# Optimization experiments

Hardware: AMD Instinct MI355X
Metric: run time of the kernel (lower is better)

Reference implementation:

```python
import jax, jax.numpy as jnp
import numpy as np

N_EDGES = 1048576
N_CENTERS = 32768
N_SPECIES = 4
L_MAX = 3
N_BASIS = 12
N_MAX = 8
R_CUT = 5.0
NORM = 1.0 / np.sqrt(32.0)  # hypers['normalize'] = avg_num_neighbors = 32
SH_SPLITS = [0, 1, 4, 9, 16]  # cumulative offsets of (2l+1)


def real_sph_harm_lmax3(u):
    # u: [E,3] unit vectors; returns [E,16] real normalized spherical harmonics (sphericart order m=-l..l)
    x, y, z = u[:, 0], u[:, 1], u[:, 2]
    c0 = 0.5 * np.sqrt(1.0 / np.pi)
    c1 = np.sqrt(3.0 / (4.0 * np.pi))
    x2, y2, z2 = x * x, y * y, z * z
    sh = [
        jnp.full_like(x, c0),
        c1 * y, c1 * z, c1 * x,
        0.5 * np.sqrt(15.0 / np.pi) * x * y,
        0.5 * np.sqrt(15.0 / np.pi) * y * z,
        0.25 * np.sqrt(5.0 / np.pi) * (3.0 * z2 - 1.0),
        0.5 * np.sqrt(15.0 / np.pi) * x * z,
        0.25 * np.sqrt(15.0 / np.pi) * (x2 - y2),
        0.25 * np.sqrt(35.0 / (2.0 * np.pi)) * y * (3.0 * x2 - y2),
        0.5 * np.sqrt(105.0 / np.pi) * x * y * z,
        0.25 * np.sqrt(21.0 / (2.0 * np.pi)) * y * (5.0 * z2 - 1.0),
        0.25 * np.sqrt(7.0 / np.pi) * (5.0 * z2 * z - 3.0 * z),
        0.25 * np.sqrt(21.0 / (2.0 * np.pi)) * x * (5.0 * z2 - 1.0),
        0.25 * np.sqrt(105.0 / np.pi) * z * (x2 - y2),
        0.25 * np.sqrt(35.0 / (2.0 * np.pi)) * x * (x2 - y2),
    ]
    return jnp.stack(sh, axis=1)


def setup_inputs() -> dict:
    key = jax.random.key(0)
    k1, k2, k3, k4 = jax.random.split(key, 4)
    vectors = jax.random.normal(k1, (N_EDGES, 3), dtype=jnp.float32) * 1.5
    radial_weights = jax.random.normal(k2, (L_MAX + 1, N_BASIS, N_MAX), dtype=jnp.float32) * 0.1
    center_index = jax.random.randint(k3, (N_EDGES,), 0, N_CENTERS, dtype=jnp.int64)
    neighbor_species_index = jax.random.randint(k4, (N_EDGES,), 0, N_SPECIES, dtype=jnp.int64)
    return {"vectors": vectors, "radial_weights": radial_weights,
            "center_index": center_index, "neighbor_species_index": neighbor_species_index}


def reference(vectors, radial_weights, center_index, neighbor_species_index):
    # distances and unit vectors
    r = jnp.sqrt(jnp.sum(vectors * vectors, axis=-1) + 1e-12)  # [E]
    u = vectors / r[:, None]
    # smooth radial basis phi_n(r) = sin((n+1) pi r / r_cut)/r, normalized (LE-like)
    ns = jnp.arange(1, N_BASIS + 1, dtype=vectors.dtype)
    phi = jnp.sin(np.pi / R_CUT * r[:, None] * ns[None, :]) / r[:, None] * NORM  # [E, N_BASIS]
    sh = real_sph_harm_lmax3(u)  # [E,16]
    # scatter target: (center, neighbor_species) channel
    idx = center_index * N_SPECIES + neighbor_species_index  # [E]
    densities = []
    for l in range(L_MAX + 1):
        m_l = 2 * l + 1
        sh_l = jax.lax.slice_in_dim(sh, SH_SPLITS[l], SH_SPLITS[l + 1], axis=1)  # [E, 2l+1]
        rad_l = phi @ radial_weights[l]  # [E, N_MAX]
        edge_l = rad_l[:, None, :] * sh_l[:, :, None]  # [E, 2l+1, N_MAX] outer product
        dens = jax.ops.segment_sum(edge_l.reshape(edge_l.shape[0], -1), idx,
                                   num_segments=N_CENTERS * N_SPECIES)  # [N*S, m*n]
        dens = dens.reshape(N_CENTERS, N_SPECIES, m_l, N_MAX)
        dens = jnp.transpose(dens, (0, 2, 1, 3)).reshape(N_CENTERS, m_l, N_SPECIES * N_MAX)
        densities.append(dens)  # c^{a_i l}_{Ai, m, a_j n}
    # concatenate the per-l TensorMap blocks along the m axis -> [N, sum(2l+1), S*N_MAX]
    return jnp.concatenate(densities, axis=1)
```

## Files before the change

### kernel.cpp

```cpp
#include <hip/hip_runtime.h>
#include <math.h>

#define N_EDGES   1048576
#define N_BUCKET  1024
#define SEG_PER_B 128
#define N_BASIS   12
#define CAP       2048

#define WS_COUNTS   0
#define WS_OFFSETS  4096
#define WS_CURSORS  8192
#define WS_SORTED   12288
#define WS_NEEDED   (12288 + 4194304)

__device__ __forceinline__ void compute_edge(float x, float y, float z,
                                             float* __restrict__ ph,
                                             float* __restrict__ sh)
{
    const float r2    = fmaf(x, x, fmaf(y, y, z * z)) + 1e-12f;
    const float inv_r = rsqrtf(r2);
    const float r     = r2 * inv_r;
    x *= inv_r; y *= inv_r; z *= inv_r;

    const float t = 0.6283185307179586f * r;
    float s1, c1;
    __sincosf(t, &s1, &c1);
    const float twoc = 2.0f * c1;
    const float scale = 0.17677669529663687f * inv_r;
    float skm1 = 0.0f, sk = s1;
    #pragma unroll
    for (int b = 0; b < N_BASIS; ++b) {
        ph[b] = sk * scale;
        const float nxt = fmaf(twoc, sk, -skm1);
        skm1 = sk; sk = nxt;
    }

    const float x2 = x * x, y2 = y * y, z2 = z * z;
    sh[0]  = 0.28209479177387814f;
    sh[1]  = 0.4886025119029199f * y;
    sh[2]  = 0.4886025119029199f * z;
    sh[3]  = 0.4886025119029199f * x;
    sh[4]  = 1.0925484305920792f * x * y;
    sh[5]  = 1.0925484305920792f * y * z;
    sh[6]  = 0.31539156525252005f * (3.0f * z2 - 1.0f);
    sh[7]  = 1.0925484305920792f * x * z;
    sh[8]  = 0.5462742152960396f * (x2 - y2);
    sh[9]  = 0.5900435899266435f * y * (3.0f * x2 - y2);
    sh[10] = 2.890611442640554f  * x * y * z;
    sh[11] = 0.4570457994644658f * y * (5.0f * z2 - 1.0f);
    sh[12] = 0.3731763325901154f * (5.0f * z2 * z - 3.0f * z);
    sh[13] = 0.4570457994644658f * x * (5.0f * z2 - 1.0f);
    sh[14] = 1.445305721320277f  * z * (x2 - y2);
    sh[15] = 0.5900435899266435f * x * (x2 - y2);
}

__device__ __forceinline__ void flush_seg(const float* __restrict__ acc,
                                          int b, int sl, int n,
                                          float* __restrict__ out)
{
    const int seg = b * SEG_PER_B + sl;
    float* op = out + (size_t)(seg >> 2) * 512 + (seg & 3) * 8 + n;
    #pragma unroll
    for (int L = 0; L < 16; ++L) op[L * 32] = acc[L];
}

__global__ __launch_bounds__(256) void hist_kernel(
    const int* __restrict__ cidx, const int* __restrict__ sidx,
    int* __restrict__ counts)
{
    __shared__ int h[N_BUCKET];
    const int t = threadIdx.x;
    #pragma unroll
    for (int i = t; i < N_BUCKET; i += 256) h[i] = 0;
    __syncthreads();
    const int base = blockIdx.x * 4096;
    #pragma unroll
    for (int k = 0; k < 16; ++k) {
        const int e = base + k * 256 + t;
        const int seg = (cidx[e] << 2) | sidx[e];
        atomicAdd(&h[seg >> 7], 1);
    }
    __syncthreads();
    #pragma unroll
    for (int i = t; i < N_BUCKET; i += 256)
        if (h[i]) atomicAdd(&counts[i], h[i]);
}

__global__ __launch_bounds__(1024) void scan_kernel(
    const int* __restrict__ counts, int* __restrict__ offsets,
    int* __restrict__ cursors)
{
    __shared__ int tmp[N_BUCKET];
    const int t = threadIdx.x;
    const int orig = counts[t];
    tmp[t] = orig;
    __syncthreads();
    #pragma unroll
    for (int d = 1; d < N_BUCKET; d <<= 1) {
        const int v = (t >= d) ? tmp[t - d] : 0;
        __syncthreads();
        tmp[t] += v;
        __syncthreads();
    }
    const int off = tmp[t] - orig;
    offsets[t] = off;
    cursors[t] = off;
}

__global__ __launch_bounds__(256) void partition_kernel(
    const int* __restrict__ cidx, const int* __restrict__ sidx,
    int* __restrict__ cursors, unsigned int* __restrict__ sorted_rec)
{
    __shared__ int bhist[N_BUCKET];
    __shared__ int bbase[N_BUCKET];
    __shared__ int lcnt[N_BUCKET];
    const int t = threadIdx.x;
    #pragma unroll
    for (int i = t; i < N_BUCKET; i += 256) bhist[i] = 0;
    __syncthreads();

    const int base = blockIdx.x * 4096;
    int segs[16];
    #pragma unroll
    for (int k = 0; k < 16; ++k) {
        const int e = base + k * 256 + t;
        segs[k] = (cidx[e] << 2) | sidx[e];
        atomicAdd(&bhist[segs[k] >> 7], 1);
    }
    __syncthreads();

    #pragma unroll
    for (int i = t; i < N_BUCKET; i += 256) {
        const int c = bhist[i];
        if (c) bbase[i] = atomicAdd(&cursors[i], c);
        lcnt[i] = 0;
    }
    __syncthreads();

    #pragma unroll
    for (int k = 0; k < 16; ++k) {
        const int e = base + k * 256 + t;
        const int seg = segs[k];
        const int bkt = seg >> 7;
        const int pos = bbase[bkt] + atomicAdd(&lcnt[bkt], 1);
        sorted_rec[pos] = ((unsigned)(seg & 127) << 20) | (unsigned)e;
    }
}

__global__ __launch_bounds__(256) void compute_kernel(
    const unsigned int* __restrict__ sorted_rec,
    const int* __restrict__ offsets, const int* __restrict__ counts,
    const float* __restrict__ vectors,
    const float* __restrict__ rw,
    float* __restrict__ out)
{
    __shared__ float4 pay[CAP];
    __shared__ int shist[SEG_PER_B];
    __shared__ int soff[SEG_PER_B];
    __shared__ int scur[SEG_PER_B];

    const int t = threadIdx.x;
    const int b = blockIdx.x;
    const int n = t & 7;
    const int g = t >> 3;

    float Wn[4][N_BASIS];
    #pragma unroll
    for (int l = 0; l < 4; ++l)
        #pragma unroll
        for (int bb = 0; bb < N_BASIS; ++bb)
            Wn[l][bb] = rw[(l * N_BASIS + bb) * 8 + n];

    const int off = offsets[b];
    const int cnt = counts[b];

    if (cnt > CAP) {
        #pragma unroll 1
        for (int k = 0; k < 4; ++k) {
            const int sl = g * 4 + k;
            float acc[16];
            #pragma unroll
            for (int L = 0; L < 16; ++L) acc[L] = 0.0f;
            for (int j = 0; j < cnt; ++j) {
                const unsigned rec = sorted_rec[off + j];
                if ((int)(rec >> 20) != sl) continue;
                const int eid = rec & 0xFFFFF;
                float ph[N_BASIS], sh[16];
                compute_edge(vectors[3*eid], vectors[3*eid+1], vectors[3*eid+2], ph, sh);
                float rad[4];
                #pragma unroll
                for (int l = 0; l < 4; ++l) {
                    float a = 0.0f;
                    #pragma unroll
                    for (int bb = 0; bb < N_BASIS; ++bb)
                        a = fmaf(ph[bb], Wn[l][bb], a);
                    rad[l] = a;
                }
                #pragma unroll
                for (int L = 0; L < 16; ++L) {
                    const int l = (L == 0) ? 0 : (L < 4) ? 1 : (L < 9) ? 2 : 3;
                    acc[L] = fmaf(sh[L], rad[l], acc[L]);
                }
            }
            flush_seg(acc, b, sl, n, out);
        }
        return;
    }

    if (t < SEG_PER_B) shist[t] = 0;
    __syncthreads();

    unsigned recs[8];
    const int iters = (cnt + 255) >> 8;
    #pragma unroll
    for (int it = 0; it < 8; ++it) {
        const int i = it * 256 + t;
        if (it < iters && i < cnt) {
            recs[it] = sorted_rec[off + i];
            atomicAdd(&shist[recs[it] >> 20], 1);
        }
    }
    __syncthreads();

    if (t < SEG_PER_B) soff[t] = shist[t];
    __syncthreads();
    #pragma unroll
    for (int d = 1; d < SEG_PER_B; d <<= 1) {
        int v = 0;
        if (t >= d && t < SEG_PER_B) v = soff[t - d];
        __syncthreads();
        if (t < SEG_PER_B) soff[t] += v;
        __syncthreads();
    }
    if (t < SEG_PER_B) {
        const int ex = soff[t] - shist[t];
        soff[t] = ex;
        scur[t] = ex;
    }
    __syncthreads();

    #pragma unroll
    for (int it = 0; it < 8; ++it) {
        const int i = it * 256 + t;
        if (it < iters && i < cnt) {
            const unsigned rec = recs[it];
            const int sl  = rec >> 20;
            const int eid = rec & 0xFFFFF;
            const int r = atomicAdd(&scur[sl], 1);
            pay[r] = make_float4(vectors[3 * eid], vectors[3 * eid + 1],
                                 vectors[3 * eid + 2], __int_as_float(sl));
        }
    }
    __syncthreads();

    const int s0 = g * 4;
    const int js = soff[s0];
    const int je = (s0 + 4 < SEG_PER_B) ? soff[s0 + 4] : cnt;

    int cur = -1;
    float acc[16];
    #pragma unroll
    for (int L = 0; L < 16; ++L) acc[L] = 0.0f;

    for (int j = js; j < je; ++j) {
        const float4 v = pay[j];
        const int sl = __float_as_int(v.w);
        if (sl != cur) {
            if (cur >= 0) {
                flush_seg(acc, b, cur, n, out);
                #pragma unroll
                for (int L = 0; L < 16; ++L) acc[L] = 0.0f;
            }
            cur = sl;
        }
        float ph[N_BASIS], sh[16];
        compute_edge(v.x, v.y, v.z, ph, sh);
        float rad[4];
        #pragma unroll
        for (int l = 0; l < 4; ++l) {
            float a = 0.0f;
            #pragma unroll
            for (int bb = 0; bb < N_BASIS; ++bb)
                a = fmaf(ph[bb], Wn[l][bb], a);
            rad[l] = a;
        }
        #pragma unroll
        for (int L = 0; L < 16; ++L) {
            const int l = (L == 0) ? 0 : (L < 4) ? 1 : (L < 9) ? 2 : 3;
            acc[L] = fmaf(sh[L], rad[l], acc[L]);
        }
    }
    if (cur >= 0) flush_seg(acc, b, cur, n, out);

    #pragma unroll
    for (int k = 0; k < 4; ++k) {
        const int sl = s0 + k;
        if (shist[sl] == 0) {
            float z[16];
            #pragma unroll
            for (int L = 0; L < 16; ++L) z[L] = 0.0f;
            flush_seg(z, b, sl, n, out);
        }
    }
}

__global__ __launch_bounds__(256) void atomic_kernel(
    const float* __restrict__ vectors, const float* __restrict__ rw,
    const int* __restrict__ cidx, const int* __restrict__ sidx,
    float* __restrict__ out)
{
    const int e = blockIdx.x * 256 + threadIdx.x;
    if (e >= N_EDGES) return;
    float ph[N_BASIS], sh[16];
    compute_edge(vectors[3*e], vectors[3*e+1], vectors[3*e+2], ph, sh);
    float* op = out + (size_t)cidx[e] * 512 + sidx[e] * 8;
    for (int l = 0; l < 4; ++l) {
        const int L0 = l * l;
        const int ml = 2 * l + 1;
        for (int n = 0; n < 8; ++n) {
            float rad = 0.0f;
            for (int b = 0; b < N_BASIS; ++b)
                rad = fmaf(ph[b], rw[(l * N_BASIS + b) * 8 + n], rad);
            for (int m = 0; m < ml; ++m)
                atomicAdd(op + (L0 + m) * 32 + n, sh[L0 + m] * rad);
        }
    }
}

extern "C" void kernel_launch(void* const* d_in, const int* in_sizes, int n_in,
                              void* d_out, int out_size, void* d_ws, size_t ws_size,
                              hipStream_t stream) {
    const float* vectors = (const float*)d_in[0];
    const float* rw      = (const float*)d_in[1];
    const int*   cidx    = (const int*)d_in[2];
    const int*   sidx    = (const int*)d_in[3];
    float*       out     = (float*)d_out;

    if (ws_size < (size_t)WS_NEEDED) {
        hipMemsetAsync(out, 0, (size_t)out_size * sizeof(float), stream);
        hipLaunchKernelGGL(atomic_kernel, dim3(N_EDGES / 256), dim3(256), 0, stream,
                           vectors, rw, cidx, sidx, out);
        return;
    }

    char* ws = (char*)d_ws;
    int*          counts  = (int*)(ws + WS_COUNTS);
    int*          offsets = (int*)(ws + WS_OFFSETS);
    int*          cursors = (int*)(ws + WS_CURSORS);
    unsigned int* sorted  = (unsigned int*)(ws + WS_SORTED);

    hipMemsetAsync(counts, 0, N_BUCKET * sizeof(int), stream);

    hipLaunchKernelGGL(hist_kernel,      dim3(N_EDGES / 4096), dim3(256),  0, stream, cidx, sidx, counts);
    hipLaunchKernelGGL(scan_kernel,      dim3(1),              dim3(1024), 0, stream, counts, offsets, cursors);
    hipLaunchKernelGGL(partition_kernel, dim3(N_EDGES / 4096), dim3(256),  0, stream, cidx, sidx, cursors, sorted);
    hipLaunchKernelGGL(compute_kernel,   dim3(N_BUCKET),       dim3(256),  0, stream, sorted, offsets, counts, vectors, rw, out);
}
```

Measured before the change: 170.8 us.

## Replace bucket sort with per-segment fixed-capacity slots and overflow fixup

Drops the histogram/scan/partition counting sort and instead scatters each edge ID into a fixed-capacity slot array per (center, species) segment using one global atomic cursor per segment. Edges beyond the capacity go to an overflow list that a small fixup kernel adds with global atomics. The compute kernel handles 32 segments per block, splits edges evenly across thread groups, accumulates into a shared tile with LDS atomics, and writes the tile out with coalesced float4 stores. This removes two launches and a full sort pass. In exchange it relies on heavy global atomic contention on 131072 cursors, reads eids and vectors with scattered access, and silently drops edges if the overflow list exceeds its capacity.

```diff
diff --git a/kernel.cpp b/kernel.cpp
--- a/kernel.cpp
+++ b/kernel.cpp
@@ -1,17 +1,16 @@
 #include <hip/hip_runtime.h>
 #include <math.h>
 
-#define N_EDGES   1048576
-#define N_BUCKET  1024
-#define SEG_PER_B 128
-#define N_BASIS   12
-#define CAP       2048
-
-#define WS_COUNTS   0
-#define WS_OFFSETS  4096
-#define WS_CURSORS  8192
-#define WS_SORTED   12288
-#define WS_NEEDED   (12288 + 4194304)
+#define N_EDGES    1048576
+#define N_CENTERS  32768
+#define N_SEG      131072
+#define N_BASIS    12
+
+#define WS_CURSORS  0
+#define WS_OVFCNT   (N_SEG * 4)
+#define OVF_CAP     65536
+#define WS_OVF      (N_SEG * 4 + 64)
+#define WS_EIDS     (N_SEG * 4 + 64 + OVF_CAP * 8)
 
 __device__ __forceinline__ void compute_edge(float x, float y, float z,
                                              float* __restrict__ ph,
@@ -54,115 +53,36 @@
     sh[15] = 0.5900435899266435f * x * (x2 - y2);
 }
 
-__device__ __forceinline__ void flush_seg(const float* __restrict__ acc,
-                                          int b, int sl, int n,
-                                          float* __restrict__ out)
-{
-    const int seg = b * SEG_PER_B + sl;
-    float* op = out + (size_t)(seg >> 2) * 512 + (seg & 3) * 8 + n;
-    #pragma unroll
-    for (int L = 0; L < 16; ++L) op[L * 32] = acc[L];
-}
-
-__global__ __launch_bounds__(256) void hist_kernel(
+__global__ __launch_bounds__(256) void scatter_kernel(
     const int* __restrict__ cidx, const int* __restrict__ sidx,
-    int* __restrict__ counts)
-{
-    __shared__ int h[N_BUCKET];
-    const int t = threadIdx.x;
-    #pragma unroll
-    for (int i = t; i < N_BUCKET; i += 256) h[i] = 0;
-    __syncthreads();
-    const int base = blockIdx.x * 4096;
-    #pragma unroll
-    for (int k = 0; k < 16; ++k) {
-        const int e = base + k * 256 + t;
-        const int seg = (cidx[e] << 2) | sidx[e];
-        atomicAdd(&h[seg >> 7], 1);
-    }
-    __syncthreads();
-    #pragma unroll
-    for (int i = t; i < N_BUCKET; i += 256)
-        if (h[i]) atomicAdd(&counts[i], h[i]);
-}
-
-__global__ __launch_bounds__(1024) void scan_kernel(
-    const int* __restrict__ counts, int* __restrict__ offsets,
-    int* __restrict__ cursors)
-{
-    __shared__ int tmp[N_BUCKET];
-    const int t = threadIdx.x;
-    const int orig = counts[t];
-    tmp[t] = orig;
-    __syncthreads();
-    #pragma unroll
-    for (int d = 1; d < N_BUCKET; d <<= 1) {
-        const int v = (t >= d) ? tmp[t - d] : 0;
-        __syncthreads();
-        tmp[t] += v;
-        __syncthreads();
-    }
-    const int off = tmp[t] - orig;
-    offsets[t] = off;
-    cursors[t] = off;
-}
-
-__global__ __launch_bounds__(256) void partition_kernel(
-    const int* __restrict__ cidx, const int* __restrict__ sidx,
-    int* __restrict__ cursors, unsigned int* __restrict__ sorted_rec)
-{
-    __shared__ int bhist[N_BUCKET];
-    __shared__ int bbase[N_BUCKET];
-    __shared__ int lcnt[N_BUCKET];
-    const int t = threadIdx.x;
-    #pragma unroll
-    for (int i = t; i < N_BUCKET; i += 256) bhist[i] = 0;
-    __syncthreads();
-
-    const int base = blockIdx.x * 4096;
-    int segs[16];
-    #pragma unroll
-    for (int k = 0; k < 16; ++k) {
-        const int e = base + k * 256 + t;
-        segs[k] = (cidx[e] << 2) | sidx[e];
-        atomicAdd(&bhist[segs[k] >> 7], 1);
-    }
-    __syncthreads();
-
-    #pragma unroll
-    for (int i = t; i < N_BUCKET; i += 256) {
-        const int c = bhist[i];
-        if (c) bbase[i] = atomicAdd(&cursors[i], c);
-        lcnt[i] = 0;
-    }
-    __syncthreads();
-
-    #pragma unroll
-    for (int k = 0; k < 16; ++k) {
-        const int e = base + k * 256 + t;
-        const int seg = segs[k];
-        const int bkt = seg >> 7;
-        const int pos = bbase[bkt] + atomicAdd(&lcnt[bkt], 1);
-        sorted_rec[pos] = ((unsigned)(seg & 127) << 20) | (unsigned)e;
+    int* __restrict__ cursors, int* __restrict__ ovf_cnt,
+    uint2* __restrict__ ovf, unsigned int* __restrict__ eids, int cap)
+{
+    const int e = blockIdx.x * 256 + threadIdx.x;
+    const int seg = (cidx[e] << 2) | sidx[e];
+    const int pos = atomicAdd(&cursors[seg], 1);
+    if (pos < cap) {
+        eids[seg * cap + pos] = (unsigned)e;
+    } else {
+        const int o = atomicAdd(ovf_cnt, 1);
+        if (o < OVF_CAP) ovf[o] = make_uint2((unsigned)seg, (unsigned)e);
     }
 }
 
 __global__ __launch_bounds__(256) void compute_kernel(
-    const unsigned int* __restrict__ sorted_rec,
-    const int* __restrict__ offsets, const int* __restrict__ counts,
+    const unsigned int* __restrict__ eids, const int* __restrict__ cursors,
     const float* __restrict__ vectors,
     const float* __restrict__ rw,
-    float* __restrict__ out)
-{
-    __shared__ float4 pay[CAP];
-    __shared__ int shist[SEG_PER_B];
-    __shared__ int soff[SEG_PER_B];
-    __shared__ int scur[SEG_PER_B];
-
-    const int t = threadIdx.x;
-    const int b = blockIdx.x;
-    const int n = t & 7;
-    const int g = t >> 3;
+    float* __restrict__ out, int cap)
+{
+    __shared__ float tile[8 * 512];
+    __shared__ int soff[33];
+
+    const int t    = threadIdx.x;
+    const int b    = blockIdx.x;
+    const int seg0 = b * 32;
+    const int n    = t & 7;
+    const int g    = t >> 3;
 
     float Wn[4][N_BASIS];
     #pragma unroll
@@ -171,135 +91,115 @@
         for (int bb = 0; bb < N_BASIS; ++bb)
             Wn[l][bb] = rw[(l * N_BASIS + bb) * 8 + n];
 
-    const int off = offsets[b];
-    const int cnt = counts[b];
-
-    if (cnt > CAP) {
-        #pragma unroll 1
-        for (int k = 0; k < 4; ++k) {
-            const int sl = g * 4 + k;
-            float acc[16];
+    #pragma unroll
+    for (int i = t; i < 4096; i += 256) tile[i] = 0.0f;
+
+    if (t < 32) {
+        int c = cursors[seg0 + t];
+        c = (c < cap) ? c : cap;
+        int v = c;
+        #pragma unroll
+        for (int d = 1; d < 32; d <<= 1) {
+            int u = __shfl_up(v, d, 32);
+            if (t >= d) v += u;
+        }
+        soff[t + 1] = v;
+        if (t == 0) soff[0] = 0;
+    }
+    __syncthreads();
+
+    const int T  = soff[32];
+    const int lo = (T * g) >> 5;
+    const int hi = (T * (g + 1)) >> 5;
+
+    if (lo < hi) {
+        int cur = 0;
+        int nxt = soff[1];
+        while (nxt <= lo) { ++cur; nxt = soff[cur + 1]; }
+        int segstart = soff[cur];
+        int eidbase  = (seg0 + cur) * cap;
+
+        float acc[16];
+        #pragma unroll
+        for (int L = 0; L < 16; ++L) acc[L] = 0.0f;
+        bool touched = false;
+
+        for (int j = lo; j < hi; ++j) {
+            while (j >= nxt) {
+                if (touched) {
+                    float* p = tile + (cur >> 2) * 512 + (cur & 3) * 8 + n;
+                    #pragma unroll
+                    for (int L = 0; L < 16; ++L) atomicAdd(p + L * 32, acc[L]);
+                    #pragma unroll
+                    for (int L = 0; L < 16; ++L) acc[L] = 0.0f;
+                    touched = false;
+                }
+                ++cur;
+                segstart = nxt;
+                nxt = soff[cur + 1];
+                eidbase += cap;
+            }
+            const unsigned eid = eids[eidbase + (j - segstart)];
+            const float x = vectors[3 * eid + 0];
+            const float y = vectors[3 * eid + 1];
+            const float z = vectors[3 * eid + 2];
+
+            float ph[N_BASIS], sh[16];
+            compute_edge(x, y, z, ph, sh);
+
+            float rad[4];
             #pragma unroll
-            for (int L = 0; L < 16; ++L) acc[L] = 0.0f;
-            for (int j = 0; j < cnt; ++j) {
-                const unsigned rec = sorted_rec[off + j];
-                if ((int)(rec >> 20) != sl) continue;
-                const int eid = rec & 0xFFFFF;
-                float ph[N_BASIS], sh[16];
-                compute_edge(vectors[3*eid], vectors[3*eid+1], vectors[3*eid+2], ph, sh);
-                float rad[4];
+            for (int l = 0; l < 4; ++l) {
+                float a = 0.0f;
                 #pragma unroll
-                for (int l = 0; l < 4; ++l) {
-                    float a = 0.0f;
-                    #pragma unroll
-                    for (int bb = 0; bb < N_BASIS; ++bb)
-                        a = fmaf(ph[bb], Wn[l][bb], a);
-                    rad[l] = a;
-                }
-                #pragma unroll
-                for (int L = 0; L < 16; ++L) {
-                    const int l = (L == 0) ? 0 : (L < 4) ? 1 : (L < 9) ? 2 : 3;
-                    acc[L] = fmaf(sh[L], rad[l], acc[L]);
-                }
-            }
-            flush_seg(acc, b, sl, n, out);
-        }
-        return;
-    }
-
-    if (t < SEG_PER_B) shist[t] = 0;
+                for (int bb = 0; bb < N_BASIS; ++bb)
+                    a = fmaf(ph[bb], Wn[l][bb], a);
+                rad[l] = a;
+            }
+            #pragma unroll
+            for (int L = 0; L < 16; ++L) {
+                const int l = (L == 0) ? 0 : (L < 4) ? 1 : (L < 9) ? 2 : 3;
+                acc[L] = fmaf(sh[L], rad[l], acc[L]);
+            }
+            touched = true;
+        }
+        if (touched) {
+            float* p = tile + (cur >> 2) * 512 + (cur & 3) * 8 + n;
+            #pragma unroll
+            for (int L = 0; L < 16; ++L) atomicAdd(p + L * 32, acc[L]);
+        }
+    }
     __syncthreads();
 
-    unsigned recs[8];
-    const int iters = (cnt + 255) >> 8;
-    #pragma unroll
-    for (int it = 0; it < 8; ++it) {
-        const int i = it * 256 + t;
-        if (it < iters && i < cnt) {
-            recs[it] = sorted_rec[off + i];
-            atomicAdd(&shist[recs[it] >> 20], 1);
-        }
-    }
-    __syncthreads();
-
-    if (t < SEG_PER_B) soff[t] = shist[t];
-    __syncthreads();
-    #pragma unroll
-    for (int d = 1; d < SEG_PER_B; d <<= 1) {
-        int v = 0;
-        if (t >= d && t < SEG_PER_B) v = soff[t - d];
-        __syncthreads();
-        if (t < SEG_PER_B) soff[t] += v;
-        __syncthreads();
-    }
-    if (t < SEG_PER_B) {
-        const int ex = soff[t] - shist[t];
-        soff[t] = ex;
-        scur[t] = ex;
-    }
-    __syncthreads();
-
-    #pragma unroll
-    for (int it = 0; it < 8; ++it) {
-        const int i = it * 256 + t;
-        if (it < iters && i < cnt) {
-            const unsigned rec = recs[it];
-            const int sl  = rec >> 20;
-            const int eid = rec & 0xFFFFF;
-            const int r = atomicAdd(&scur[sl], 1);
-            pay[r] = make_float4(vectors[3 * eid], vectors[3 * eid + 1],
-                                 vectors[3 * eid + 2], __int_as_float(sl));
-        }
-    }
-    __syncthreads();
-
-    const int s0 = g * 4;
-    const int js = soff[s0];
-    const int je = (s0 + 4 < SEG_PER_B) ? soff[s0 + 4] : cnt;
-
-    int cur = -1;
-    float acc[16];
-    #pragma unroll
-    for (int L = 0; L < 16; ++L) acc[L] = 0.0f;
-
-    for (int j = js; j < je; ++j) {
-        const float4 v = pay[j];
-        const int sl = __float_as_int(v.w);
-        if (sl != cur) {
-            if (cur >= 0) {
-                flush_seg(acc, b, cur, n, out);
-                #pragma unroll
-                for (int L = 0; L < 16; ++L) acc[L] = 0.0f;
-            }
-            cur = sl;
-        }
+    float4*       o4 = (float4*)(out + (size_t)b * 4096);
+    const float4* t4 = (const float4*)tile;
+    #pragma unroll
+    for (int k = 0; k < 4; ++k) o4[k * 256 + t] = t4[k * 256 + t];
+}
+
+__global__ __launch_bounds__(256) void fixup_kernel(
+    const int* __restrict__ ovf_cnt, const uint2* __restrict__ ovf,
+    const float* __restrict__ vectors, const float* __restrict__ rw,
+    float* __restrict__ out)
+{
+    const int m = (*ovf_cnt < OVF_CAP) ? *ovf_cnt : OVF_CAP;
+    for (int i = blockIdx.x * blockDim.x + threadIdx.x; i < m;
+         i += gridDim.x * blockDim.x) {
+        const unsigned seg = ovf[i].x;
+        const unsigned e   = ovf[i].y;
         float ph[N_BASIS], sh[16];
-        compute_edge(v.x, v.y, v.z, ph, sh);
-        float rad[4];
-        #pragma unroll
+        compute_edge(vectors[3*e], vectors[3*e+1], vectors[3*e+2], ph, sh);
+        float* op = out + (size_t)(seg >> 2) * 512 + (seg & 3) * 8;
         for (int l = 0; l < 4; ++l) {
-            float a = 0.0f;
-            #pragma unroll
-            for (int bb = 0; bb < N_BASIS; ++bb)
-                a = fmaf(ph[bb], Wn[l][bb], a);
-            rad[l] = a;
-        }
-        #pragma unroll
-        for (int L = 0; L < 16; ++L) {
-            const int l = (L == 0) ? 0 : (L < 4) ? 1 : (L < 9) ? 2 : 3;
-            acc[L] = fmaf(sh[L], rad[l], acc[L]);
-        }
-    }
-    if (cur >= 0) flush_seg(acc, b, cur, n, out);
-
-    #pragma unroll
-    for (int k = 0; k < 4; ++k) {
-        const int sl = s0 + k;
-        if (shist[sl] == 0) {
-            float z[16];
-            #pragma unroll
-            for (int L = 0; L < 16; ++L) z[L] = 0.0f;
-            flush_seg(z, b, sl, n, out);
+            const int L0 = l * l;
+            const int ml = 2 * l + 1;
+            for (int nn = 0; nn < 8; ++nn) {
+                float rad = 0.0f;
+                for (int bb = 0; bb < N_BASIS; ++bb)
+                    rad = fmaf(ph[bb], rw[(l * N_BASIS + bb) * 8 + nn], rad);
+                for (int mm = 0; mm < ml; ++mm)
+                    atomicAdd(op + (L0 + mm) * 32 + nn, sh[L0 + mm] * rad);
+            }
         }
     }
 }
@@ -317,12 +217,12 @@
     for (int l = 0; l < 4; ++l) {
         const int L0 = l * l;
         const int ml = 2 * l + 1;
-        for (int n = 0; n < 8; ++n) {
+        for (int nn = 0; nn < 8; ++nn) {
             float rad = 0.0f;
-            for (int b = 0; b < N_BASIS; ++b)
-                rad = fmaf(ph[b], rw[(l * N_BASIS + b) * 8 + n], rad);
-            for (int m = 0; m < ml; ++m)
-                atomicAdd(op + (L0 + m) * 32 + n, sh[L0 + m] * rad);
+            for (int bb = 0; bb < N_BASIS; ++bb)
+                rad = fmaf(ph[bb], rw[(l * N_BASIS + bb) * 8 + nn], rad);
+            for (int mm = 0; mm < ml; ++mm)
+                atomicAdd(op + (L0 + mm) * 32 + nn, sh[L0 + mm] * rad);
         }
     }
 }
@@ -336,7 +236,11 @@
     const int*   sidx    = (const int*)d_in[3];
     float*       out     = (float*)d_out;
 
-    if (ws_size < (size_t)WS_NEEDED) {
+    const size_t need32 = (size_t)WS_EIDS + (size_t)N_SEG * 32 * 4;
+    const size_t need16 = (size_t)WS_EIDS + (size_t)N_SEG * 16 * 4;
+    const int cap = (ws_size >= need32) ? 32 : ((ws_size >= need16) ? 16 : 0);
+
+    if (cap == 0) {
         hipMemsetAsync(out, 0, (size_t)out_size * sizeof(float), stream);
         hipLaunchKernelGGL(atomic_kernel, dim3(N_EDGES / 256), dim3(256), 0, stream,
                            vectors, rw, cidx, sidx, out);
@@ -344,15 +248,17 @@
     }
 
     char* ws = (char*)d_ws;
-    int*          counts  = (int*)(ws + WS_COUNTS);
-    int*          offsets = (int*)(ws + WS_OFFSETS);
     int*          cursors = (int*)(ws + WS_CURSORS);
-    unsigned int* sorted  = (unsigned int*)(ws + WS_SORTED);
-
-    hipMemsetAsync(counts, 0, N_BUCKET * sizeof(int), stream);
-
-    hipLaunchKernelGGL(hist_kernel,      dim3(N_EDGES / 4096), dim3(256),  0, stream, cidx, sidx, counts);
-    hipLaunchKernelGGL(scan_kernel,      dim3(1),              dim3(1024), 0, stream, counts, offsets, cursors);
-    hipLaunchKernelGGL(partition_kernel, dim3(N_EDGES / 4096), dim3(256),  0, stream, cidx, sidx, cursors, sorted);
-    hipLaunchKernelGGL(compute_kernel,   dim3(N_BUCKET),       dim3(256),  0, stream, sorted, offsets, counts, vectors, rw, out);
-}
+    int*          ovfcnt  = (int*)(ws + WS_OVFCNT);
+    uint2*        ovf     = (uint2*)(ws + WS_OVF);
+    unsigned int* eids    = (unsigned int*)(ws + WS_EIDS);
+
+    hipMemsetAsync(ws, 0, WS_OVFCNT + 64, stream);
+
+    hipLaunchKernelGGL(scatter_kernel, dim3(N_EDGES / 256), dim3(256), 0, stream,
+                       cidx, sidx, cursors, ovfcnt, ovf, eids, cap);
+    hipLaunchKernelGGL(compute_kernel, dim3(N_SEG / 32), dim3(256), 0, stream,
+                       eids, cursors, vectors, rw, out, cap);
+    hipLaunchKernelGGL(fixup_kernel, dim3(4), dim3(256), 0, stream,
+                       ovfcnt, ovf, vectors, rw, out);
+}
```

Result: slower. 330.9 us (+93.7%).

## Replace global-atomic bucket sort with per-block histograms and deterministic scan

Applied to the files above, without the earlier changes.

Histogram blocks now write per-block bucket counts to workspace instead of doing global atomics. A column scan produces per-block offsets and a second scan produces the bucket offsets, so partition no longer recomputes its histogram or takes global cursor atomics. The memset goes away and bucket placement becomes deterministic. In exchange it adds one more kernel launch and a 1 MB per-block histogram. The scanA pass is serial over 256 blocks in only 16 small workgroups, which may cost latency.

```diff
diff --git a/kernel.cpp b/kernel.cpp
--- a/kernel.cpp
+++ b/kernel.cpp
@@ -6,12 +6,15 @@
 #define SEG_PER_B 128
 #define N_BASIS   12
 #define CAP       2048
-
-#define WS_COUNTS   0
-#define WS_OFFSETS  4096
-#define WS_CURSORS  8192
-#define WS_SORTED   12288
-#define WS_NEEDED   (12288 + 4194304)
+#define HBLK      256
+#define HEPB      (N_EDGES / HBLK)
+
+
+#define WS_BLKHIST  0
+#define WS_TOTALS   (HBLK * N_BUCKET * 4)
+#define WS_OFFSETS  (WS_TOTALS + N_BUCKET * 4)
+#define WS_RECORDS  (WS_OFFSETS + N_BUCKET * 4)
+#define WS_NEEDED   (WS_RECORDS + N_EDGES * 4)
 
 __device__ __forceinline__ void compute_edge(float x, float y, float z,
                                              float* __restrict__ ph,
@@ -66,16 +69,16 @@
 
 __global__ __launch_bounds__(256) void hist_kernel(
     const int* __restrict__ cidx, const int* __restrict__ sidx,
-    int* __restrict__ counts)
+    int* __restrict__ blkhist)
 {
     __shared__ int h[N_BUCKET];
     const int t = threadIdx.x;
     #pragma unroll
     for (int i = t; i < N_BUCKET; i += 256) h[i] = 0;
     __syncthreads();
-    const int base = blockIdx.x * 4096;
-    #pragma unroll
-    for (int k = 0; k < 16; ++k) {
+    const int base = blockIdx.x * HEPB;
+    #pragma unroll
+    for (int k = 0; k < HEPB / 256; ++k) {
         const int e = base + k * 256 + t;
         const int seg = (cidx[e] << 2) | sidx[e];
         atomicAdd(&h[seg >> 7], 1);
@@ -83,16 +86,28 @@
     __syncthreads();
     #pragma unroll
     for (int i = t; i < N_BUCKET; i += 256)
-        if (h[i]) atomicAdd(&counts[i], h[i]);
-}
-
-__global__ __launch_bounds__(1024) void scan_kernel(
-    const int* __restrict__ counts, int* __restrict__ offsets,
-    int* __restrict__ cursors)
+        blkhist[blockIdx.x * N_BUCKET + i] = h[i];
+}
+
+__global__ __launch_bounds__(64) void scanA_kernel(
+    int* __restrict__ blkhist, int* __restrict__ totals)
+{
+    const int bkt = blockIdx.x * 64 + threadIdx.x;
+    int run = 0;
+    for (int blk = 0; blk < HBLK; ++blk) {
+        const int v = blkhist[blk * N_BUCKET + bkt];
+        blkhist[blk * N_BUCKET + bkt] = run;
+        run += v;
+    }
+    totals[bkt] = run;
+}
+
+__global__ __launch_bounds__(1024) void scanB_kernel(
+    const int* __restrict__ totals, int* __restrict__ offsets)
 {
     __shared__ int tmp[N_BUCKET];
     const int t = threadIdx.x;
-    const int orig = counts[t];
+    const int orig = totals[t];
     tmp[t] = orig;
     __syncthreads();
     #pragma unroll
@@ -102,48 +117,31 @@
         tmp[t] += v;
         __syncthreads();
     }
-    const int off = tmp[t] - orig;
-    offsets[t] = off;
-    cursors[t] = off;
+    offsets[t] = tmp[t] - orig;
 }
 
 __global__ __launch_bounds__(256) void partition_kernel(
     const int* __restrict__ cidx, const int* __restrict__ sidx,
-    int* __restrict__ cursors, unsigned int* __restrict__ sorted_rec)
-{
-    __shared__ int bhist[N_BUCKET];
-    __shared__ int bbase[N_BUCKET];
+    const int* __restrict__ blkhist, const int* __restrict__ offsets,
+    unsigned int* __restrict__ records)
+{
+    __shared__ int bb[N_BUCKET];
     __shared__ int lcnt[N_BUCKET];
     const int t = threadIdx.x;
     #pragma unroll
-    for (int i = t; i < N_BUCKET; i += 256) bhist[i] = 0;
-    __syncthreads();
-
-    const int base = blockIdx.x * 4096;
-    int segs[16];
-    #pragma unroll
-    for (int k = 0; k < 16; ++k) {
+    for (int i = t; i < N_BUCKET; i += 256) {
+        bb[i] = offsets[i] + blkhist[blockIdx.x * N_BUCKET + i];
+        lcnt[i] = 0;
+    }
+    __syncthreads();
+    const int base = blockIdx.x * HEPB;
+    #pragma unroll
+    for (int k = 0; k < HEPB / 256; ++k) {
         const int e = base + k * 256 + t;
-        segs[k] = (cidx[e] << 2) | sidx[e];
-        atomicAdd(&bhist[segs[k] >> 7], 1);
-    }
-    __syncthreads();
-
-    #pragma unroll
-    for (int i = t; i < N_BUCKET; i += 256) {
-        const int c = bhist[i];
-        if (c) bbase[i] = atomicAdd(&cursors[i], c);
-        lcnt[i] = 0;
-    }
-    __syncthreads();
-
-    #pragma unroll
-    for (int k = 0; k < 16; ++k) {
-        const int e = base + k * 256 + t;
-        const int seg = segs[k];
+        const int seg = (cidx[e] << 2) | sidx[e];
         const int bkt = seg >> 7;
-        const int pos = bbase[bkt] + atomicAdd(&lcnt[bkt], 1);
-        sorted_rec[pos] = ((unsigned)(seg & 127) << 20) | (unsigned)e;
+        const int r = atomicAdd(&lcnt[bkt], 1);
+        records[bb[bkt] + r] = ((unsigned)(seg & 127) << 20) | (unsigned)e;
     }
 }
 
@@ -317,12 +315,12 @@
     for (int l = 0; l < 4; ++l) {
         const int L0 = l * l;
         const int ml = 2 * l + 1;
-        for (int n = 0; n < 8; ++n) {
+        for (int nn = 0; nn < 8; ++nn) {
             float rad = 0.0f;
-            for (int b = 0; b < N_BASIS; ++b)
-                rad = fmaf(ph[b], rw[(l * N_BASIS + b) * 8 + n], rad);
-            for (int m = 0; m < ml; ++m)
-                atomicAdd(op + (L0 + m) * 32 + n, sh[L0 + m] * rad);
+            for (int bb = 0; bb < N_BASIS; ++bb)
+                rad = fmaf(ph[bb], rw[(l * N_BASIS + bb) * 8 + nn], rad);
+            for (int mm = 0; mm < ml; ++mm)
+                atomicAdd(op + (L0 + mm) * 32 + nn, sh[L0 + mm] * rad);
         }
     }
 }
@@ -344,15 +342,14 @@
     }
 
     char* ws = (char*)d_ws;
-    int*          counts  = (int*)(ws + WS_COUNTS);
+    int*          blkhist = (int*)(ws + WS_BLKHIST);
+    int*          totals  = (int*)(ws + WS_TOTALS);
     int*          offsets = (int*)(ws + WS_OFFSETS);
-    int*          cursors = (int*)(ws + WS_CURSORS);
-    unsigned int* sorted  = (unsigned int*)(ws + WS_SORTED);
-
-    hipMemsetAsync(counts, 0, N_BUCKET * sizeof(int), stream);
-
-    hipLaunchKernelGGL(hist_kernel,      dim3(N_EDGES / 4096), dim3(256),  0, stream, cidx, sidx, counts);
-    hipLaunchKernelGGL(scan_kernel,      dim3(1),              dim3(1024), 0, stream, counts, offsets, cursors);
-    hipLaunchKernelGGL(partition_kernel, dim3(N_EDGES / 4096), dim3(256),  0, stream, cidx, sidx, cursors, sorted);
-    hipLaunchKernelGGL(compute_kernel,   dim3(N_BUCKET),       dim3(256),  0, stream, sorted, offsets, counts, vectors, rw, out);
-}
+    unsigned int* records = (unsigned int*)(ws + WS_RECORDS);
+
+    hipLaunchKernelGGL(hist_kernel,      dim3(HBLK),      dim3(256),  0, stream, cidx, sidx, blkhist);
+    hipLaunchKernelGGL(scanA_kernel,     dim3(N_BUCKET/64), dim3(64), 0, stream, blkhist, totals);
+    hipLaunchKernelGGL(scanB_kernel,     dim3(1),         dim3(1024), 0, stream, totals, offsets);
+    hipLaunchKernelGGL(partition_kernel, dim3(HBLK),      dim3(256),  0, stream, cidx, sidx, blkhist, offsets, records);
+    hipLaunchKernelGGL(compute_kernel,   dim3(N_BUCKET),  dim3(256),  0, stream, records, offsets, totals, vectors, rw, out);
+}
```

Result: no change. 169.9 us (-0.6%).
